# Kernel optimization log

Measured on AMD Instinct MI355X. Metric: run time of the kernel, lower is better.

The kernel has to match this reference:

```python
import jax, jax.numpy as jnp
import numpy as np

DIL = 1  # dilation (== padding for 3x3 stride-1)
KK = 9   # 3x3 kernel points


def setup_inputs() -> dict:
    key = jax.random.key(0)
    k1, k2, k3, k4 = jax.random.split(key, 4)
    B, C, H, W = 8, 64, 128, 128
    Cout = 64
    x = jax.random.normal(k1, (B, C, H, W), jnp.float32)
    # offset/mask conv: nn.Conv2d default init scale-ish; keep offsets moderate
    w_off = jax.random.normal(k2, (27, C, 3, 3), jnp.float32) * 0.02
    b_off = jax.random.uniform(k3, (27,), jnp.float32, -0.05, 0.05)
    # c2_msra_fill: std = sqrt(2 / (fan_in + fan_out)), fan_in = C*9
    std = float(np.sqrt(2.0 / (C * 9 + Cout)))
    w_dcn = jax.random.normal(k4, (Cout, C, 3, 3), jnp.float32) * std
    return {"x": x, "w_off": w_off, "b_off": b_off, "w_dcn": w_dcn}


def _conv3x3(x, w, b, dil):
    out = jax.lax.conv_general_dilated(
        x, w, window_strides=(1, 1), padding=[(dil, dil), (dil, dil)],
        rhs_dilation=(dil, dil), dimension_numbers=("NCHW", "OIHW", "NCHW"))
    return out + b[None, :, None, None]


def reference(x, w_off, b_off, w_dcn):
    B, C, H, W = x.shape
    Cout = w_dcn.shape[0]
    # offset/mask conv, chunk into offset_x / offset_y / mask, cat offsets
    om = _conv3x3(x, w_off, b_off, DIL)                  # [B,27,H,W]
    off_x, off_y, mask = jnp.split(om, 3, axis=1)        # each [B,9,H,W]
    offset = jnp.concatenate([off_x, off_y], axis=1)     # [B,18,H,W]
    mask = jax.nn.sigmoid(mask)                          # [B,9,H,W]
    # mmcv DCNv2 layout: offset channel 2k = dy_k, 2k+1 = dx_k
    off = offset.reshape(B, KK, 2, H, W)
    dy, dx = off[:, :, 0], off[:, :, 1]                  # [B,9,H,W]
    # base sampling grid: p = out_pos - pad + k*dil (stride 1, pad = dil)
    ky, kx = jnp.meshgrid(jnp.arange(3), jnp.arange(3), indexing="ij")
    ky = ky.reshape(KK).astype(jnp.float32)
    kx = kx.reshape(KK).astype(jnp.float32)
    base_y = (jnp.arange(H, dtype=jnp.float32)[None, :, None]
              - DIL + ky[:, None, None] * DIL)           # [9,H,1]
    base_x = (jnp.arange(W, dtype=jnp.float32)[None, None, :]
              - DIL + kx[:, None, None] * DIL)           # [9,1,W]
    py = dy + base_y[None]                               # [B,9,H,W]
    px = dx + base_x[None]
    # bilinear sample with zero padding outside the image
    y0 = jnp.floor(py)
    x0 = jnp.floor(px)
    xf = x.reshape(B, C, H * W)
    sampled = jnp.zeros((B, C, KK, H, W), x.dtype)
    for oy in (0.0, 1.0):
        for ox in (0.0, 1.0):
            yi = y0 + oy
            xi = x0 + ox
            wgt = (1.0 - jnp.abs(py - yi)) * (1.0 - jnp.abs(px - xi))
            valid = (yi >= 0) & (yi < H) & (xi >= 0) & (xi < W)
            yc = jnp.clip(yi, 0, H - 1).astype(jnp.int32)
            xc = jnp.clip(xi, 0, W - 1).astype(jnp.int32)
            idx = (yc * W + xc).reshape(B, KK * H * W)
            vals = jax.vmap(lambda f, i: jnp.take(f, i, axis=1))(xf, idx)
            vals = vals.reshape(B, C, KK, H, W)
            sampled = sampled + vals * (wgt * valid)[:, None]
    sampled = sampled * mask[:, None]                    # modulation
    # weighted reduction == conv with gathered patches
    out = jnp.einsum("bckhw,ock->bohw", sampled, w_dcn.reshape(Cout, C, KK))
    return out
```

## Files before the change

kernel.cpp:

```cpp
#include <hip/hip_runtime.h>
#include <math.h>

#define B_  8
#define C_  64
#define H_  128
#define W_  128
#define KK_ 9
#define CO_ 64
#define HW_ (H_*W_)
#define CK_ 576

typedef _Float16 f16x8 __attribute__((ext_vector_type(8)));
typedef _Float16 h2    __attribute__((ext_vector_type(2)));
typedef __attribute__((ext_vector_type(4))) float f32x4;

__device__ inline unsigned pkrtz(float a, float b){
    auto v = __builtin_amdgcn_cvt_pkrtz(a, b);
    union{decltype(v) h; unsigned u;} c; c.h = v; return c.u;
}
__device__ inline h2 u2h(unsigned u){ union{unsigned x; h2 h;} c; c.x = u; return c.h; }
__device__ inline unsigned h2u(h2 v){ union{h2 h; unsigned u;} c; c.h = v; return c.u; }
__device__ inline unsigned short f2h(float f){
    _Float16 h = (_Float16)f;
    union{_Float16 h; unsigned short s;} c; c.h = h; return c.s;
}
__device__ inline h2 bcast_lo(unsigned u){ return u2h(__builtin_amdgcn_perm(u, u, 0x01000100)); }
__device__ inline h2 bcast_hi(unsigned u){ return u2h(__builtin_amdgcn_perm(u, u, 0x03020302)); }

__global__ __launch_bounds__(256) void transpose_prep(
    const float* __restrict__ x, unsigned short* __restrict__ xt,
    const float* __restrict__ w_dcn, const float* __restrict__ w_off,
    unsigned short* __restrict__ w_bf, unsigned short* __restrict__ wA)
{
    __shared__ unsigned tb[64 * 33];
    if (blockIdx.x >= B_ * 256) {
        int i = (blockIdx.x - B_ * 256) * 256 + threadIdx.x;
        if (i < 64 * CK_) {
            int o = i / CK_, r = i % CK_;
            int tap = r >> 6, c = r & 63;
            w_bf[i] = f2h(w_dcn[o * CK_ + c * 9 + tap]);
        } else {
            int j = i - 64 * CK_;
            int o = j / CK_, r = j % CK_;
            int tap = r >> 6, c = r & 63;
            float v = (o < 27) ? w_off[o * CK_ + c * 9 + tap] : 0.f;
            wA[j] = f2h(v);
        }
        return;
    }
    int b = blockIdx.x >> 8;
    int pixbase = (blockIdx.x & 255) * 64;
    int t = threadIdx.x;
    #pragma unroll
    for (int i = 0; i < 2; ++i) {
        int idx = i * 256 + t;
        int cp = idx >> 4;
        int p4 = (idx & 15) * 4;
        const float* r0 = x + ((size_t)(b * C_) + 2 * cp    ) * HW_ + pixbase + p4;
        const float* r1 = x + ((size_t)(b * C_) + 2 * cp + 1) * HW_ + pixbase + p4;
        float4 f0 = *(const float4*)r0;
        float4 f1 = *(const float4*)r1;
        tb[(p4 + 0) * 33 + cp] = pkrtz(f0.x, f1.x);
        tb[(p4 + 1) * 33 + cp] = pkrtz(f0.y, f1.y);
        tb[(p4 + 2) * 33 + cp] = pkrtz(f0.z, f1.z);
        tb[(p4 + 3) * 33 + cp] = pkrtz(f0.w, f1.w);
    }
    __syncthreads();
    unsigned* xo = (unsigned*)xt + ((size_t)b * HW_ + pixbase) * 32;
    #pragma unroll
    for (int i = 0; i < 2; ++i) {
        int idx = i * 256 + t;
        int pix = idx >> 3, j = idx & 7;
        uint4 v;
        v.x = tb[pix * 33 + j * 4 + 0];
        v.y = tb[pix * 33 + j * 4 + 1];
        v.z = tb[pix * 33 + j * 4 + 2];
        v.w = tb[pix * 33 + j * 4 + 3];
        *(uint4*)(xo + pix * 32 + j * 4) = v;
    }
}


#define PXB 128
#define ROWB (66 * PXB)
#define SSTRB 144
#define SBUF (64 * SSTRB)

__global__ __launch_bounds__(256, 4) void dcn17(
    const unsigned short* __restrict__ xt,
    const unsigned short* __restrict__ wA,
    const float* __restrict__ b_off,
    const unsigned short* __restrict__ w_bf,
    float* __restrict__ out)
{
    __shared__ __align__(16) unsigned char uni[25600];
    __shared__ uint2 scr_w[576];
    __shared__ int   scr_o[576];
    unsigned char* xrow = uni;
    float* om = (float*)uni;
    unsigned char* sS = uni;

    int tile = blockIdx.x;
    int b  = tile >> 8;
    int p0 = (tile & 255) * 64;
    int y  = p0 >> 7;
    int x0 = p0 & 127;
    int t  = threadIdx.x;
    int lane = t & 63, w = t >> 6;
    int m = lane & 15, q = lane >> 4;

    const unsigned short* xbr = xt + (size_t)(b * HW_) * 64;

    for (int i = t; i < 3 * 66 * 8; i += 256) {
        int r = i / 528;
        int rem = i - r * 528;
        int c = rem >> 3;
        int g = rem & 7;
        int yy = y - 1 + r;
        int xx = x0 - 1 + c;
        uint4 v = {0, 0, 0, 0};
        if (yy >= 0 && yy < H_ && xx >= 0 && xx < W_)
            v = *(const uint4*)(xbr + ((size_t)yy * W_ + xx) * 64 + g * 8);
        *(uint4*)(xrow + r * ROWB + c * PXB + ((g ^ (c & 7)) << 4)) = v;
    }
    __syncthreads();

    {
        int o0c = (w & 1) * 16;
        int pxh = (w >> 1) * 32;

        f32x4 accc[2] = {};
        #pragma unroll
        for (int ky = 0; ky < 3; ++ky) {
            #pragma unroll
            for (int kx = 0; kx < 3; ++kx) {
                int s2 = (ky * 3 + kx) * 2;
                f16x8 A0 = *(const f16x8*)(wA + (o0c + m) * CK_ + s2 * 32 + q * 8);
                f16x8 A1 = *(const f16x8*)(wA + (o0c + m) * CK_ + (s2 + 1) * 32 + q * 8);
                #pragma unroll
                for (int nt = 0; nt < 2; ++nt) {
                    int c = pxh + nt * 16 + m + kx;
                    const unsigned char* p = xrow + ky * ROWB + c * PXB;
                    int off0 = (q ^ (c & 7)) << 4;
                    f16x8 b0 = *(const f16x8*)(p + off0);
                    f16x8 b1 = *(const f16x8*)(p + (off0 ^ 64));
                    accc[nt] = __builtin_amdgcn_mfma_f32_16x16x32_f16(A0, b0, accc[nt], 0, 0, 0);
                    accc[nt] = __builtin_amdgcn_mfma_f32_16x16x32_f16(A1, b1, accc[nt], 0, 0, 0);
                }
            }
        }
        __syncthreads();
        #pragma unroll
        for (int nt = 0; nt < 2; ++nt) {
            #pragma unroll
            for (int r = 0; r < 4; ++r) {
                int j = o0c + q * 4 + r;
                if (j < 27)
                    om[j * 65 + pxh + nt * 16 + m] = accc[nt][r] + b_off[j];
            }
        }
    }
    __syncthreads();

    for (int i = t; i < 576; i += 256) {
        int k = i >> 6, sp = i & 63;
        float dy = om[(2 * k)     * 65 + sp];
        float dx = om[(2 * k + 1) * 65 + sp];
        float mk = 1.f / (1.f + __expf(-om[(18 + k) * 65 + sp]));
        float py = dy + (float)(y - 1 + k / 3);
        float px = dx + (float)(x0 + sp - 1 + k % 3);
        float fy = floorf(py), fx = floorf(px);
        int iy = (int)fy, ix = (int)fx;
        float ay = py - fy, ax = px - fx;
        float wy0 = (iy >= 0  && iy < H_)     ? (1.f - ay) : 0.f;
        float wy1 = (iy >= -1 && iy < H_ - 1) ? ay         : 0.f;
        float wx0 = (ix >= 0  && ix < W_)     ? (1.f - ax) : 0.f;
        float wx1 = (ix >= -1 && ix < W_ - 1) ? ax         : 0.f;
        int iy0 = min(max(iy, 0), H_ - 1);
        int iy1 = min(max(iy + 1, 0), H_ - 1);
        int ix0 = min(max(ix, 0), W_ - 1);
        int ix1 = min(max(ix + 1, 0), W_ - 1);
        float w00 = wy0*wx0*mk, w01 = wy0*wx1*mk, w10 = wy1*wx0*mk, w11 = wy1*wx1*mk;
        uint2 wv;
        wv.x = pkrtz(w00, w01);
        wv.y = pkrtz(w10, w11);
        scr_w[i] = wv;
        int off00 = (iy0 * W_ + ix0) * 128;
        scr_o[i] = off00 | ((ix1 != ix0) << 22) | ((iy1 != iy0) << 23);
    }

    int o0 = w * 16;
    __syncthreads();

    int cq = lane & 7;
    int g  = lane >> 3;
    const unsigned char* xb = (const unsigned char*)xbr;
    f32x4 acc[4] = {};
    int piB = w * 8 + g;

#define PROD(K) do {                                                        \
        const int k_ = (K);                                                 \
        uint2 wC_ = {}; int pC_ = 0;                                        \
        if (k_ + 2 < 18) {                                                  \
            int P = piB + (k_ + 2) * 32;                                    \
            wC_ = scr_w[P]; pC_ = scr_o[P];                                 \
        }                                                                   \
        uint4 n00 = {}, n01 = {}, n10 = {}, n11 = {};                       \
        if (k_ + 1 < 18) {                                                  \
            const unsigned char* a0 = xb + (pB_ & 0x3FFFFF) + cq * 16;      \
            int dxb = (pB_ >> 15) & 128;                                    \
            int dyb = (pB_ >> 9)  & 16384;                                  \
            n00 = *(const uint4*)(a0);                                      \
            n01 = *(const uint4*)(a0 + dxb);                                \
            n10 = *(const uint4*)(a0 + dyb);                                \
            n11 = *(const uint4*)(a0 + dyb + dxb);                          \
        }                                                                   \
        h2 w00 = bcast_lo(wA_.x), w01 = bcast_hi(wA_.x);                    \
        h2 w10 = bcast_lo(wA_.y), w11 = bcast_hi(wA_.y);                    \
        uint4 o4; h2 r;                                                     \
        r = w00*u2h(a00.x) + w01*u2h(a01.x) + w10*u2h(a10.x) + w11*u2h(a11.x); o4.x = h2u(r); \
        r = w00*u2h(a00.y) + w01*u2h(a01.y) + w10*u2h(a10.y) + w11*u2h(a11.y); o4.y = h2u(r); \
        r = w00*u2h(a00.z) + w01*u2h(a01.z) + w10*u2h(a10.z) + w11*u2h(a11.z); o4.z = h2u(r); \
        r = w00*u2h(a00.w) + w01*u2h(a01.w) + w10*u2h(a10.w) + w11*u2h(a11.w); o4.w = h2u(r); \
        int sp_ = (piB + (k_ & 1) * 32) & 63;                               \
        *(uint4*)&sS[((k_ >> 1) & 1) * SBUF + sp_ * SSTRB + cq * 16] = o4;  \
        wA_ = wB_; wB_ = wC_; pB_ = pC_;                                    \
        a00 = n00; a01 = n01; a10 = n10; a11 = n11;                         \
    } while (0)

    uint2 wA_, wB_; int pB_;
    uint4 a00, a01, a10, a11;
    {
        wA_ = scr_w[piB];      int oo = scr_o[piB];
        wB_ = scr_w[piB + 32]; pB_ = scr_o[piB + 32];
        const unsigned char* a0 = xb + (oo & 0x3FFFFF) + cq * 16;
        int dxb = (oo >> 15) & 128;
        int dyb = (oo >> 9)  & 16384;
        a00 = *(const uint4*)(a0);
        a01 = *(const uint4*)(a0 + dxb);
        a10 = *(const uint4*)(a0 + dyb);
        a11 = *(const uint4*)(a0 + dyb + dxb);
    }

    f16x8 AfC0 = *(const f16x8*)(w_bf + (o0 + m) * CK_ + 0 * 32 + q * 8);
    f16x8 AfC1 = *(const f16x8*)(w_bf + (o0 + m) * CK_ + 1 * 32 + q * 8);

    PROD(0); PROD(1);
    __syncthreads();

    #pragma unroll
    for (int tp = 0; tp < 9; ++tp) {
        f16x8 AfN0, AfN1;
        if (tp < 8) {
            PROD(2 * tp + 2);
            PROD(2 * tp + 3);
            AfN0 = *(const f16x8*)(w_bf + (o0 + m) * CK_ + (2 * tp + 2) * 32 + q * 8);
            AfN1 = *(const f16x8*)(w_bf + (o0 + m) * CK_ + (2 * tp + 3) * 32 + q * 8);
        }
        #pragma unroll
        for (int nt = 0; nt < 4; ++nt) {
            f16x8 bb0 = *(const f16x8*)&sS[(tp & 1) * SBUF + (nt * 16 + m) * SSTRB + q * 16];
            acc[nt] = __builtin_amdgcn_mfma_f32_16x16x32_f16(AfC0, bb0, acc[nt], 0, 0, 0);
        }
        #pragma unroll
        for (int nt = 0; nt < 4; ++nt) {
            f16x8 bb1 = *(const f16x8*)&sS[(tp & 1) * SBUF + (nt * 16 + m) * SSTRB + 64 + q * 16];
            acc[nt] = __builtin_amdgcn_mfma_f32_16x16x32_f16(AfC1, bb1, acc[nt], 0, 0, 0);
        }
        if (tp < 8) {
            __syncthreads();
            AfC0 = AfN0; AfC1 = AfN1;
        }
    }
#undef PROD

    #pragma unroll
    for (int nt = 0; nt < 4; ++nt) {
        #pragma unroll
        for (int r = 0; r < 4; ++r) {
            int o = o0 + q * 4 + r;
            out[((size_t)(b * CO_ + o)) * HW_ + p0 + nt * 16 + m] = acc[nt][r];
        }
    }
}

extern "C" void kernel_launch(void* const* d_in, const int* in_sizes, int n_in,
                              void* d_out, int out_size, void* d_ws, size_t ws_size,
                              hipStream_t stream)
{
    const float* x     = (const float*)d_in[0];
    const float* w_off = (const float*)d_in[1];
    const float* b_off = (const float*)d_in[2];
    const float* w_dcn = (const float*)d_in[3];
    float* out = (float*)d_out;

    unsigned short* xt   = (unsigned short*)d_ws;
    unsigned short* w_bf = xt + (size_t)B_ * HW_ * 64;
    unsigned short* wA   = w_bf + 64 * CK_;

    transpose_prep<<<B_ * 256 + 216, 256, 0, stream>>>(x, xt, w_dcn, w_off, w_bf, wA);
    dcn17<<<B_ * 256, 256, 0, stream>>>(xt, wA, b_off, w_bf, out);
}
```

Baseline: 146.7 us.

## Halve pixel tile to 32 per block with 128 threads and 2x2 MFMA warp tiles

Each block now handles 32 output pixels with 2 waves instead of 64 pixels with 4 waves, which doubles the block count and halves shared memory per block. In the offset conv, each wave covers 16 offset channels across all 32 pixels. In the main GEMM, each wave computes 32 output channels by 32 pixels, reusing each B fragment for two A fragments. The intent is better occupancy and load balance with fewer bytes loaded from LDS per MFMA. In exchange, each block recomputes a larger share of halo rows and reloads the weights more often.

```diff
diff --git a/kernel.cpp b/kernel.cpp
--- a/kernel.cpp
+++ b/kernel.cpp
@@ -82,27 +82,27 @@
 
 
 #define PXB 128
-#define ROWB (66 * PXB)
+#define ROWB (34 * PXB)
 #define SSTRB 144
-#define SBUF (64 * SSTRB)
-
-__global__ __launch_bounds__(256, 4) void dcn17(
+#define SBUF (32 * SSTRB)
+
+__global__ __launch_bounds__(128, 4) void dcn18(
     const unsigned short* __restrict__ xt,
     const unsigned short* __restrict__ wA,
     const float* __restrict__ b_off,
     const unsigned short* __restrict__ w_bf,
     float* __restrict__ out)
 {
-    __shared__ __align__(16) unsigned char uni[25600];
-    __shared__ uint2 scr_w[576];
-    __shared__ int   scr_o[576];
+    __shared__ __align__(16) unsigned char uni[13056];
+    __shared__ uint2 scr_w[288];
+    __shared__ int   scr_o[288];
     unsigned char* xrow = uni;
     float* om = (float*)uni;
     unsigned char* sS = uni;
 
     int tile = blockIdx.x;
-    int b  = tile >> 8;
-    int p0 = (tile & 255) * 64;
+    int b  = tile >> 9;
+    int p0 = (tile & 511) * 32;
     int y  = p0 >> 7;
     int x0 = p0 & 127;
     int t  = threadIdx.x;
@@ -111,9 +111,9 @@
 
     const unsigned short* xbr = xt + (size_t)(b * HW_) * 64;
 
-    for (int i = t; i < 3 * 66 * 8; i += 256) {
-        int r = i / 528;
-        int rem = i - r * 528;
+    for (int i = t; i < 3 * 34 * 8; i += 128) {
+        int r = i / 272;
+        int rem = i - r * 272;
         int c = rem >> 3;
         int g = rem & 7;
         int yy = y - 1 + r;
@@ -126,8 +126,7 @@
     __syncthreads();
 
     {
-        int o0c = (w & 1) * 16;
-        int pxh = (w >> 1) * 32;
+        int o0c = w * 16;
 
         f32x4 accc[2] = {};
         #pragma unroll
@@ -139,7 +138,7 @@
                 f16x8 A1 = *(const f16x8*)(wA + (o0c + m) * CK_ + (s2 + 1) * 32 + q * 8);
                 #pragma unroll
                 for (int nt = 0; nt < 2; ++nt) {
-                    int c = pxh + nt * 16 + m + kx;
+                    int c = nt * 16 + m + kx;
                     const unsigned char* p = xrow + ky * ROWB + c * PXB;
                     int off0 = (q ^ (c & 7)) << 4;
                     f16x8 b0 = *(const f16x8*)(p + off0);
@@ -156,17 +155,17 @@
             for (int r = 0; r < 4; ++r) {
                 int j = o0c + q * 4 + r;
                 if (j < 27)
-                    om[j * 65 + pxh + nt * 16 + m] = accc[nt][r] + b_off[j];
+                    om[j * 33 + nt * 16 + m] = accc[nt][r] + b_off[j];
             }
         }
     }
     __syncthreads();
 
-    for (int i = t; i < 576; i += 256) {
-        int k = i >> 6, sp = i & 63;
-        float dy = om[(2 * k)     * 65 + sp];
-        float dx = om[(2 * k + 1) * 65 + sp];
-        float mk = 1.f / (1.f + __expf(-om[(18 + k) * 65 + sp]));
+    for (int i = t; i < 288; i += 128) {
+        int k = i >> 5, sp = i & 31;
+        float dy = om[(2 * k)     * 33 + sp];
+        float dx = om[(2 * k + 1) * 33 + sp];
+        float mk = 1.f / (1.f + __expf(-om[(18 + k) * 33 + sp]));
         float py = dy + (float)(y - 1 + k / 3);
         float px = dx + (float)(x0 + sp - 1 + k % 3);
         float fy = floorf(py), fx = floorf(px);
@@ -189,7 +188,7 @@
         scr_o[i] = off00 | ((ix1 != ix0) << 22) | ((iy1 != iy0) << 23);
     }
 
-    int o0 = w * 16;
+    int o0 = w * 32;
     __syncthreads();
 
     int cq = lane & 7;
@@ -202,7 +201,7 @@
         const int k_ = (K);                                                 \
         uint2 wC_ = {}; int pC_ = 0;                                        \
         if (k_ + 2 < 18) {                                                  \
-            int P = piB + (k_ + 2) * 32;                                    \
+            int P = piB + (k_ + 2) * 16;                                    \
             wC_ = scr_w[P]; pC_ = scr_o[P];                                 \
         }                                                                   \
         uint4 n00 = {}, n01 = {}, n10 = {}, n11 = {};                       \
@@ -222,7 +221,7 @@
         r = w00*u2h(a00.y) + w01*u2h(a01.y) + w10*u2h(a10.y) + w11*u2h(a11.y); o4.y = h2u(r); \
         r = w00*u2h(a00.z) + w01*u2h(a01.z) + w10*u2h(a10.z) + w11*u2h(a11.z); o4.z = h2u(r); \
         r = w00*u2h(a00.w) + w01*u2h(a01.w) + w10*u2h(a10.w) + w11*u2h(a11.w); o4.w = h2u(r); \
-        int sp_ = (piB + (k_ & 1) * 32) & 63;                               \
+        int sp_ = piB + (k_ & 1) * 16;                                      \
         *(uint4*)&sS[((k_ >> 1) & 1) * SBUF + sp_ * SSTRB + cq * 16] = o4;  \
         wA_ = wB_; wB_ = wC_; pB_ = pC_;                                    \
         a00 = n00; a01 = n01; a10 = n10; a11 = n11;                         \
@@ -232,7 +231,7 @@
     uint4 a00, a01, a10, a11;
     {
         wA_ = scr_w[piB];      int oo = scr_o[piB];
-        wB_ = scr_w[piB + 32]; pB_ = scr_o[piB + 32];
+        wB_ = scr_w[piB + 16]; pB_ = scr_o[piB + 16];
         const unsigned char* a0 = xb + (oo & 0x3FFFFF) + cq * 16;
         int dxb = (oo >> 15) & 128;
         int dyb = (oo >> 9)  & 16384;
@@ -242,44 +241,54 @@
         a11 = *(const uint4*)(a0 + dyb + dxb);
     }
 
-    f16x8 AfC0 = *(const f16x8*)(w_bf + (o0 + m) * CK_ + 0 * 32 + q * 8);
-    f16x8 AfC1 = *(const f16x8*)(w_bf + (o0 + m) * CK_ + 1 * 32 + q * 8);
+    f16x8 AfC00 = *(const f16x8*)(w_bf + (o0 +      m) * CK_ + 0 * 32 + q * 8);
+    f16x8 AfC01 = *(const f16x8*)(w_bf + (o0 +      m) * CK_ + 1 * 32 + q * 8);
+    f16x8 AfC10 = *(const f16x8*)(w_bf + (o0 + 16 + m) * CK_ + 0 * 32 + q * 8);
+    f16x8 AfC11 = *(const f16x8*)(w_bf + (o0 + 16 + m) * CK_ + 1 * 32 + q * 8);
 
     PROD(0); PROD(1);
     __syncthreads();
 
     #pragma unroll
     for (int tp = 0; tp < 9; ++tp) {
-        f16x8 AfN0, AfN1;
+        f16x8 AfN00, AfN01, AfN10, AfN11;
         if (tp < 8) {
             PROD(2 * tp + 2);
             PROD(2 * tp + 3);
-            AfN0 = *(const f16x8*)(w_bf + (o0 + m) * CK_ + (2 * tp + 2) * 32 + q * 8);
-            AfN1 = *(const f16x8*)(w_bf + (o0 + m) * CK_ + (2 * tp + 3) * 32 + q * 8);
-        }
-        #pragma unroll
-        for (int nt = 0; nt < 4; ++nt) {
-            f16x8 bb0 = *(const f16x8*)&sS[(tp & 1) * SBUF + (nt * 16 + m) * SSTRB + q * 16];
-            acc[nt] = __builtin_amdgcn_mfma_f32_16x16x32_f16(AfC0, bb0, acc[nt], 0, 0, 0);
-        }
-        #pragma unroll
-        for (int nt = 0; nt < 4; ++nt) {
-            f16x8 bb1 = *(const f16x8*)&sS[(tp & 1) * SBUF + (nt * 16 + m) * SSTRB + 64 + q * 16];
-            acc[nt] = __builtin_amdgcn_mfma_f32_16x16x32_f16(AfC1, bb1, acc[nt], 0, 0, 0);
+            AfN00 = *(const f16x8*)(w_bf + (o0 +      m) * CK_ + (2 * tp + 2) * 32 + q * 8);
+            AfN01 = *(const f16x8*)(w_bf + (o0 +      m) * CK_ + (2 * tp + 3) * 32 + q * 8);
+            AfN10 = *(const f16x8*)(w_bf + (o0 + 16 + m) * CK_ + (2 * tp + 2) * 32 + q * 8);
+            AfN11 = *(const f16x8*)(w_bf + (o0 + 16 + m) * CK_ + (2 * tp + 3) * 32 + q * 8);
+        }
+        const unsigned char* sb = sS + (tp & 1) * SBUF;
+        #pragma unroll
+        for (int nt = 0; nt < 2; ++nt) {
+            f16x8 bb = *(const f16x8*)&sb[(nt * 16 + m) * SSTRB + q * 16];
+            acc[0 * 2 + nt] = __builtin_amdgcn_mfma_f32_16x16x32_f16(AfC00, bb, acc[0 * 2 + nt], 0, 0, 0);
+            acc[1 * 2 + nt] = __builtin_amdgcn_mfma_f32_16x16x32_f16(AfC10, bb, acc[1 * 2 + nt], 0, 0, 0);
+        }
+        #pragma unroll
+        for (int nt = 0; nt < 2; ++nt) {
+            f16x8 bb = *(const f16x8*)&sb[(nt * 16 + m) * SSTRB + 64 + q * 16];
+            acc[0 * 2 + nt] = __builtin_amdgcn_mfma_f32_16x16x32_f16(AfC01, bb, acc[0 * 2 + nt], 0, 0, 0);
+            acc[1 * 2 + nt] = __builtin_amdgcn_mfma_f32_16x16x32_f16(AfC11, bb, acc[1 * 2 + nt], 0, 0, 0);
         }
         if (tp < 8) {
             __syncthreads();
-            AfC0 = AfN0; AfC1 = AfN1;
+            AfC00 = AfN00; AfC01 = AfN01; AfC10 = AfN10; AfC11 = AfN11;
         }
     }
 #undef PROD
 
     #pragma unroll
-    for (int nt = 0; nt < 4; ++nt) {
-        #pragma unroll
-        for (int r = 0; r < 4; ++r) {
-            int o = o0 + q * 4 + r;
-            out[((size_t)(b * CO_ + o)) * HW_ + p0 + nt * 16 + m] = acc[nt][r];
+    for (int jo = 0; jo < 2; ++jo) {
+        #pragma unroll
+        for (int nt = 0; nt < 2; ++nt) {
+            #pragma unroll
+            for (int r = 0; r < 4; ++r) {
+                int o = o0 + jo * 16 + q * 4 + r;
+                out[((size_t)(b * CO_ + o)) * HW_ + p0 + nt * 16 + m] = acc[jo * 2 + nt][r];
+            }
         }
     }
 }
@@ -299,5 +308,5 @@
     unsigned short* wA   = w_bf + 64 * CK_;
 
     transpose_prep<<<B_ * 256 + 216, 256, 0, stream>>>(x, xt, w_dcn, w_off, w_bf, wA);
-    dcn17<<<B_ * 256, 256, 0, stream>>>(xt, wA, b_off, w_bf, out);
-}
+    dcn18<<<B_ * 512, 128, 0, stream>>>(xt, wA, b_off, w_bf, out);
+}
```

After: 162.6 us. +10.8%, slower.
